# Kernel tuning notes

Hardware: AMD Instinct MI355X
Metric: run time of the kernel (lower is better)

The kernel has to match this reference:

```python
import jax, jax.numpy as jnp
import numpy as np

BETA = 0.25

def setup_inputs() -> dict:
    key = jax.random.key(0)
    k1, k2 = jax.random.split(key)
    z = jax.random.normal(k1, (4096, 64, 64), dtype=jnp.float32)
    codebooks = jax.random.normal(k2, (64, 256, 64), dtype=jnp.float32)
    return {"z": z, "codebooks": codebooks}

def reference(z, codebooks):
    # z: (B, M, d); codebooks: (M, K, d)
    B, M, d = z.shape
    # squared distances (B, M, K) via ||z||^2 - 2 z.c + ||c||^2 (avoids (B,M,K,d) blowup)
    z2 = jnp.sum(z * z, axis=-1)                      # (B, M)
    c2 = jnp.sum(codebooks * codebooks, axis=-1)      # (M, K)
    zc = jnp.einsum('bmd,mkd->bmk', z, codebooks)     # (B, M, K)
    distances = z2[:, :, None] - 2.0 * zc + c2[None]  # (B, M, K)
    encoding_indices = jnp.argmin(distances, axis=-1) # (B, M) int
    # per-subspace codebook gather: codebooks[m, idx[b, m], :]
    quantized_raw = codebooks[jnp.arange(M)[None, :], encoding_indices]  # (B, M, d)
    # straight-through estimator
    quantized = z + jax.lax.stop_gradient(quantized_raw - z)
    q_loss = (BETA * jnp.mean((jax.lax.stop_gradient(quantized) - z) ** 2)
              + jnp.mean((quantized - jax.lax.stop_gradient(z)) ** 2))
    return quantized, encoding_indices, q_loss
```

## Files before the change

kernel.cpp:

```cpp
#include <hip/hip_runtime.h>

#define IDX_BASE 16777216UL
#define LOSS_IDX 17039360UL
#define EPS2 0.02f

typedef float4 f4;
typedef _Float16 half8 __attribute__((ext_vector_type(8)));
typedef float f32x4 __attribute__((ext_vector_type(4)));

static __device__ __forceinline__ unsigned umax(unsigned a, unsigned b) { return a > b ? a : b; }
static __device__ __forceinline__ unsigned umin(unsigned a, unsigned b) { return a < b ? a : b; }
static __device__ __forceinline__ unsigned f2mono(float s) {
    unsigned u = __float_as_uint(s);
    return u ^ (unsigned)(((int)u >> 31) | 0x80000000);
}
static __device__ __forceinline__ float mono2f(unsigned v) {
    return __uint_as_float(v ^ (((unsigned)((int)(~v) >> 31)) | 0x80000000u));
}

__device__ __forceinline__ void gload_lds16(const float* g, float* s) {
    __builtin_amdgcn_global_load_lds(
        (const __attribute__((address_space(1))) unsigned int*)g,
        (__attribute__((address_space(3))) unsigned int*)s, 16, 0, 0);
}

__global__ __launch_bounds__(256) void pq_frag(const float* __restrict__ cb,
                                               half8* __restrict__ fragbuf,
                                               float* __restrict__ c2) {
    int bx = blockIdx.x, tid = threadIdx.x;
    int m = bx >> 2, sub = bx & 3;
    int w = tid >> 6, lane = tid & 63, lh = lane >> 4, l15 = lane & 15;
    const float* cbm = cb + (size_t)m * (256 * 64);
    half8* fbm = fragbuf + (size_t)m * (16 * 4 * 64);
    int tile = w * 4 + sub;
    int code = tile * 16 + l15;
    const float* crow = cbm + code * 64 + lh * 8;
    float ss = 0.f;
    #pragma unroll
    for (int s = 0; s < 2; ++s) {
        f4 a = *reinterpret_cast<const f4*>(crow + s * 32);
        f4 b = *reinterpret_cast<const f4*>(crow + s * 32 + 4);
        float v[8] = {a.x, a.y, a.z, a.w, b.x, b.y, b.z, b.w};
        half8 hi, lo;
        #pragma unroll
        for (int e = 0; e < 8; ++e) {
            _Float16 h = (_Float16)v[e];
            hi[e] = h; lo[e] = (_Float16)(v[e] - (float)h);
            ss = fmaf(v[e], v[e], ss);
        }
        fbm[(tile * 4 + s * 2 + 0) * 64 + lane] = hi;
        fbm[(tile * 4 + s * 2 + 1) * 64 + lane] = lo;
    }
    ss += __shfl_xor(ss, 16, 64);
    ss += __shfl_xor(ss, 32, 64);
    if (lh == 0) c2[m * 256 + code] = ss;
}

__global__ __launch_bounds__(256, 3) void pq_main(
    const float* __restrict__ z, const float* __restrict__ cb,
    const float* __restrict__ c2ws, const half8* __restrict__ fragbuf,
    float* __restrict__ out, float* __restrict__ partial)
{
    __shared__ f4       sZ4[128 * 16];
    __shared__ unsigned sK1[4 * 128];
    __shared__ unsigned sK2[4 * 128];
    __shared__ int      sBest[128];
    __shared__ float    sW[4];

    const int tid = threadIdx.x, bx = blockIdx.x;
    const int m = ((bx & 7) << 3) | ((bx >> 3) & 7);
    const int chunk = bx >> 6;
    const int w = tid >> 6, lane = tid & 63;
    const int lh = lane >> 4, l15 = lane & 15;
    const unsigned payBase = 255u - (unsigned)(w * 64 + lh * 4);

    const float* __restrict__ cbm = cb + (size_t)m * (256 * 64);
    const f4* cb4m = reinterpret_cast<const f4*>(cbm);

    #pragma unroll
    for (int i = 0; i < 8; ++i) {
        int unit = i * 256 + w * 64 + lane;
        int row = unit >> 4, c4 = unit & 15;
        int c4p = c4 ^ (row & 7);
        const float* src = z + ((size_t)(chunk * 128 + row) * 64 + m) * 64 + c4p * 4;
        gload_lds16(src, (float*)&sZ4[i * 256 + w * 64]);
    }

    const half8* __restrict__ fb = fragbuf + (size_t)m * (16 * 4 * 64);
    half8 ah[4][2], al[4][2];
    #pragma unroll
    for (int t = 0; t < 4; ++t) {
        #pragma unroll
        for (int s = 0; s < 2; ++s) {
            ah[t][s] = fb[((w * 4 + t) * 4 + s * 2 + 0) * 64 + lane];
            al[t][s] = fb[((w * 4 + t) * 4 + s * 2 + 1) * 64 + lane];
        }
    }
    const f4* __restrict__ c2t = reinterpret_cast<const f4*>(c2ws + m * 256);
    f32x4 c2i[4];
    #pragma unroll
    for (int t = 0; t < 4; ++t) {
        f4 cv = c2t[(w * 4 + t) * 4 + lh];
        c2i[t][0] = -0.5f*cv.x; c2i[t][1] = -0.5f*cv.y;
        c2i[t][2] = -0.5f*cv.z; c2i[t][3] = -0.5f*cv.w;
    }

    __syncthreads();

    #pragma unroll 1
    for (int rtp = 0; rtp < 4; ++rtp) {
        half8 bh0[2], bl0[2], bh1[2], bl1[2];
        #pragma unroll
        for (int h = 0; h < 2; ++h) {
            const int row = (rtp * 2 + h) * 16 + l15;
            const int swz = row & 7;
            const f4* zr = &sZ4[row * 16];
            const int c0 = lh << 1;
            f4 a0 = zr[(c0)     ^ swz];
            f4 a1 = zr[(c0 + 1) ^ swz];
            f4 a2 = zr[(c0 + 8) ^ swz];
            f4 a3 = zr[(c0 + 9) ^ swz];
            float v0[8] = {a0.x,a0.y,a0.z,a0.w,a1.x,a1.y,a1.z,a1.w};
            float v1[8] = {a2.x,a2.y,a2.z,a2.w,a3.x,a3.y,a3.z,a3.w};
            #pragma unroll
            for (int e = 0; e < 8; ++e) {
                _Float16 h0 = (_Float16)v0[e];
                bh0[h][e] = h0; bl0[h][e] = (_Float16)(v0[e] - (float)h0);
                _Float16 h1 = (_Float16)v1[e];
                bh1[h][e] = h1; bl1[h][e] = (_Float16)(v1[e] - (float)h1);
            }
        }
        unsigned K1[2] = {0u, 0u}, K2[2] = {0u, 0u};
        #pragma unroll
        for (int t = 0; t < 4; ++t) {
            const unsigned pb = payBase - (unsigned)(t * 16);
            #pragma unroll
            for (int h = 0; h < 2; ++h) {
                f32x4 acc = c2i[t];
                acc = __builtin_amdgcn_mfma_f32_16x16x32_f16(ah[t][0], bh0[h], acc, 0, 0, 0);
                acc = __builtin_amdgcn_mfma_f32_16x16x32_f16(ah[t][1], bh1[h], acc, 0, 0, 0);
                acc = __builtin_amdgcn_mfma_f32_16x16x32_f16(ah[t][0], bl0[h], acc, 0, 0, 0);
                acc = __builtin_amdgcn_mfma_f32_16x16x32_f16(ah[t][1], bl1[h], acc, 0, 0, 0);
                acc = __builtin_amdgcn_mfma_f32_16x16x32_f16(al[t][0], bh0[h], acc, 0, 0, 0);
                acc = __builtin_amdgcn_mfma_f32_16x16x32_f16(al[t][1], bh1[h], acc, 0, 0, 0);
                unsigned kk0 = (f2mono(acc[0]) & 0xFFFFFF00u) | (pb - 0u);
                unsigned kk1 = (f2mono(acc[1]) & 0xFFFFFF00u) | (pb - 1u);
                unsigned kk2 = (f2mono(acc[2]) & 0xFFFFFF00u) | (pb - 2u);
                unsigned kk3 = (f2mono(acc[3]) & 0xFFFFFF00u) | (pb - 3u);
                unsigned a  = umax(kk0, kk1), b2 = umin(kk0, kk1);
                unsigned c  = umax(kk2, kk3), d  = umin(kk2, kk3);
                unsigned t1 = umax(a, c);
                unsigned t2 = umax(umin(a, c), umax(b2, d));
                K2[h] = umax(umax(K2[h], t2), umin(K1[h], t1));
                K1[h] = umax(K1[h], t1);
            }
        }
        #pragma unroll
        for (int h = 0; h < 2; ++h) {
            #pragma unroll
            for (int off = 16; off <= 32; off <<= 1) {
                unsigned o1 = (unsigned)__shfl_xor((int)K1[h], off, 64);
                unsigned o2 = (unsigned)__shfl_xor((int)K2[h], off, 64);
                K2[h] = umax(umax(K2[h], o2), umin(K1[h], o1));
                K1[h] = umax(K1[h], o1);
            }
            if (lane < 16) {
                int r2 = (rtp * 2 + h) * 16 + lane;
                sK1[w * 128 + r2] = K1[h];
                sK2[w * 128 + r2] = K2[h];
            }
        }
    }
    __syncthreads();

    if (tid < 128) {
        unsigned G1 = 0u, G2 = 0u;
        #pragma unroll
        for (int w2 = 0; w2 < 4; ++w2) {
            unsigned k1w = sK1[w2 * 128 + tid];
            unsigned k2w = sK2[w2 * 128 + tid];
            G2 = umax(umax(G2, k2w), umin(G1, k1w));
            G1 = umax(G1, k1w);
        }
        float s1 = mono2f(G1 & 0xFFFFFF00u);
        float s2 = mono2f(G2 & 0xFFFFFF00u);
        sBest[tid] = (s1 - s2 < EPS2) ? -1 : (int)(255u - (G1 & 0xFFu));
    }
    __syncthreads();

    for (int row = w; row < 128; row += 4) {
        if (sBest[row] >= 0) continue;
        int swz = row & 7;
        float bs = -1e30f; int bk = 0;
        #pragma unroll 1
        for (int j = 0; j < 4; ++j) {
            int k = j * 64 + lane;
            float s = -0.5f * c2ws[m * 256 + k];
            #pragma unroll
            for (int d4 = 0; d4 < 16; ++d4) {
                f4 cvv = cb4m[k * 16 + d4];
                f4 zz  = sZ4[row * 16 + (d4 ^ swz)];
                s = fmaf(zz.x, cvv.x, s); s = fmaf(zz.y, cvv.y, s);
                s = fmaf(zz.z, cvv.z, s); s = fmaf(zz.w, cvv.w, s);
            }
            if (s > bs) { bs = s; bk = k; }
        }
        #pragma unroll
        for (int off = 1; off < 64; off <<= 1) {
            float ov = __shfl_xor(bs, off, 64);
            int   ok = __shfl_xor(bk, off, 64);
            if (ov > bs || (ov == bs && ok < bk)) { bs = ov; bk = ok; }
        }
        if (lane == 0) sBest[row] = bk;
    }
    __syncthreads();

    float lsum = 0.f;
    {
        int row = tid >> 1, h = tid & 1;
        int k = sBest[row];
        int b = chunk * 128 + row;
        int swz = row & 7;
        const f4* q4 = cb4m + (size_t)k * 16 + h * 8;
        f4*       o4 = reinterpret_cast<f4*>(out + ((size_t)b * 64 + m) * 64) + h * 8;
        float l0 = 0.f, l1 = 0.f;
        #pragma unroll
        for (int c = 0; c < 8; ++c) {
            f4 qv = q4[c];
            f4 zv = sZ4[row * 16 + (((h << 3) + c) ^ swz)];
            o4[c] = qv;
            float d0 = qv.x - zv.x, d1 = qv.y - zv.y, d2 = qv.z - zv.z, d3 = qv.w - zv.w;
            l0 = fmaf(d0, d0, l0); l1 = fmaf(d1, d1, l1);
            l0 = fmaf(d2, d2, l0); l1 = fmaf(d3, d3, l1);
        }
        lsum = l0 + l1;
    }
    if (tid < 128)
        out[IDX_BASE + (size_t)(chunk * 128 + tid) * 64 + m] = (float)sBest[tid];
    #pragma unroll
    for (int off = 1; off < 64; off <<= 1) lsum += __shfl_xor(lsum, off, 64);
    if (lane == 0) sW[w] = lsum;
    __syncthreads();
    if (tid == 0) partial[bx] = (sW[0] + sW[1]) + (sW[2] + sW[3]);
}

__global__ __launch_bounds__(256) void pq_loss(const float* __restrict__ partial,
                                               float* __restrict__ out)
{
    __shared__ float sW[4];
    float s = 0.f;
    #pragma unroll
    for (int i = 0; i < 8; ++i) s += partial[threadIdx.x + i * 256];
    #pragma unroll
    for (int off = 1; off < 64; off <<= 1) s += __shfl_xor(s, off, 64);
    if ((threadIdx.x & 63) == 0) sW[threadIdx.x >> 6] = s;
    __syncthreads();
    if (threadIdx.x == 0)
        out[LOSS_IDX] = ((sW[0] + sW[1]) + (sW[2] + sW[3])) * (1.25f / 16777216.0f);
}

extern "C" void kernel_launch(void* const* d_in, const int* in_sizes, int n_in,
                              void* d_out, int out_size, void* d_ws, size_t ws_size,
                              hipStream_t stream) {
    const float* zp  = (const float*)d_in[0];
    const float* cbp = (const float*)d_in[1];
    float* outp = (float*)d_out;
    float* c2ws = (float*)d_ws;
    half8* frag = (half8*)((float*)d_ws + 16384);
    float* part = (float*)d_ws + 16384 + 1048576;

    pq_frag<<<dim3(256),  dim3(256), 0, stream>>>(cbp, frag, c2ws);
    pq_main<<<dim3(2048), dim3(256), 0, stream>>>(zp, cbp, c2ws, frag, outp, part);
    pq_loss<<<dim3(1),    dim3(256), 0, stream>>>(part, outp);
}
```

Before: 84.58 us.

## Stage z as precomputed fp16 hi/lo MFMA fragments in LDS instead of fp32

Measured after the change: 94.01 us. +11.1%, slower.

```diff
diff --git a/kernel.cpp b/kernel.cpp
--- a/kernel.cpp
+++ b/kernel.cpp
@@ -16,12 +16,6 @@
 }
 static __device__ __forceinline__ float mono2f(unsigned v) {
     return __uint_as_float(v ^ (((unsigned)((int)(~v) >> 31)) | 0x80000000u));
-}
-
-__device__ __forceinline__ void gload_lds16(const float* g, float* s) {
-    __builtin_amdgcn_global_load_lds(
-        (const __attribute__((address_space(1))) unsigned int*)g,
-        (__attribute__((address_space(3))) unsigned int*)s, 16, 0, 0);
 }
 
 __global__ __launch_bounds__(256) void pq_frag(const float* __restrict__ cb,
@@ -61,7 +55,7 @@
     const float* __restrict__ c2ws, const half8* __restrict__ fragbuf,
     float* __restrict__ out, float* __restrict__ partial)
 {
-    __shared__ f4       sZ4[128 * 16];
+    __shared__ half8    sZfrag[8 * 4 * 64];
     __shared__ unsigned sK1[4 * 128];
     __shared__ unsigned sK2[4 * 128];
     __shared__ int      sBest[128];
@@ -78,12 +72,28 @@
     const f4* cb4m = reinterpret_cast<const f4*>(cbm);
 
     #pragma unroll
-    for (int i = 0; i < 8; ++i) {
-        int unit = i * 256 + w * 64 + lane;
-        int row = unit >> 4, c4 = unit & 15;
-        int c4p = c4 ^ (row & 7);
-        const float* src = z + ((size_t)(chunk * 128 + row) * 64 + m) * 64 + c4p * 4;
-        gload_lds16(src, (float*)&sZ4[i * 256 + w * 64]);
+    for (int i = 0; i < 2; ++i) {
+        int rt = w * 2 + i;
+        size_t rh = (size_t)(chunk * 128 + rt * 16 + l15);
+        const float* zb = z + (rh * 64 + m) * 64 + lh * 8;
+        f4 p0 = *reinterpret_cast<const f4*>(zb);
+        f4 p1 = *reinterpret_cast<const f4*>(zb + 4);
+        f4 p2 = *reinterpret_cast<const f4*>(zb + 32);
+        f4 p3 = *reinterpret_cast<const f4*>(zb + 36);
+        float v0[8] = {p0.x,p0.y,p0.z,p0.w,p1.x,p1.y,p1.z,p1.w};
+        float v1[8] = {p2.x,p2.y,p2.z,p2.w,p3.x,p3.y,p3.z,p3.w};
+        half8 h0, l0, h1, l1;
+        #pragma unroll
+        for (int e = 0; e < 8; ++e) {
+            _Float16 a = (_Float16)v0[e];
+            h0[e] = a; l0[e] = (_Float16)(v0[e] - (float)a);
+            _Float16 b = (_Float16)v1[e];
+            h1[e] = b; l1[e] = (_Float16)(v1[e] - (float)b);
+        }
+        sZfrag[rt * 256 +   0 + lane] = h0;
+        sZfrag[rt * 256 +  64 + lane] = l0;
+        sZfrag[rt * 256 + 128 + lane] = h1;
+        sZfrag[rt * 256 + 192 + lane] = l1;
     }
 
     const half8* __restrict__ fb = fragbuf + (size_t)m * (16 * 4 * 64);
@@ -108,67 +118,41 @@
     __syncthreads();
 
     #pragma unroll 1
-    for (int rtp = 0; rtp < 4; ++rtp) {
-        half8 bh0[2], bl0[2], bh1[2], bl1[2];
-        #pragma unroll
-        for (int h = 0; h < 2; ++h) {
-            const int row = (rtp * 2 + h) * 16 + l15;
-            const int swz = row & 7;
-            const f4* zr = &sZ4[row * 16];
-            const int c0 = lh << 1;
-            f4 a0 = zr[(c0)     ^ swz];
-            f4 a1 = zr[(c0 + 1) ^ swz];
-            f4 a2 = zr[(c0 + 8) ^ swz];
-            f4 a3 = zr[(c0 + 9) ^ swz];
-            float v0[8] = {a0.x,a0.y,a0.z,a0.w,a1.x,a1.y,a1.z,a1.w};
-            float v1[8] = {a2.x,a2.y,a2.z,a2.w,a3.x,a3.y,a3.z,a3.w};
-            #pragma unroll
-            for (int e = 0; e < 8; ++e) {
-                _Float16 h0 = (_Float16)v0[e];
-                bh0[h][e] = h0; bl0[h][e] = (_Float16)(v0[e] - (float)h0);
-                _Float16 h1 = (_Float16)v1[e];
-                bh1[h][e] = h1; bl1[h][e] = (_Float16)(v1[e] - (float)h1);
-            }
-        }
-        unsigned K1[2] = {0u, 0u}, K2[2] = {0u, 0u};
+    for (int rt = 0; rt < 8; ++rt) {
+        const half8* zf = &sZfrag[rt * 256 + lane];
+        half8 bh0 = zf[0], bl0 = zf[64], bh1 = zf[128], bl1 = zf[192];
+        unsigned K1 = 0u, K2 = 0u;
         #pragma unroll
         for (int t = 0; t < 4; ++t) {
             const unsigned pb = payBase - (unsigned)(t * 16);
-            #pragma unroll
-            for (int h = 0; h < 2; ++h) {
-                f32x4 acc = c2i[t];
-                acc = __builtin_amdgcn_mfma_f32_16x16x32_f16(ah[t][0], bh0[h], acc, 0, 0, 0);
-                acc = __builtin_amdgcn_mfma_f32_16x16x32_f16(ah[t][1], bh1[h], acc, 0, 0, 0);
-                acc = __builtin_amdgcn_mfma_f32_16x16x32_f16(ah[t][0], bl0[h], acc, 0, 0, 0);
-                acc = __builtin_amdgcn_mfma_f32_16x16x32_f16(ah[t][1], bl1[h], acc, 0, 0, 0);
-                acc = __builtin_amdgcn_mfma_f32_16x16x32_f16(al[t][0], bh0[h], acc, 0, 0, 0);
-                acc = __builtin_amdgcn_mfma_f32_16x16x32_f16(al[t][1], bh1[h], acc, 0, 0, 0);
-                unsigned kk0 = (f2mono(acc[0]) & 0xFFFFFF00u) | (pb - 0u);
-                unsigned kk1 = (f2mono(acc[1]) & 0xFFFFFF00u) | (pb - 1u);
-                unsigned kk2 = (f2mono(acc[2]) & 0xFFFFFF00u) | (pb - 2u);
-                unsigned kk3 = (f2mono(acc[3]) & 0xFFFFFF00u) | (pb - 3u);
-                unsigned a  = umax(kk0, kk1), b2 = umin(kk0, kk1);
-                unsigned c  = umax(kk2, kk3), d  = umin(kk2, kk3);
-                unsigned t1 = umax(a, c);
-                unsigned t2 = umax(umin(a, c), umax(b2, d));
-                K2[h] = umax(umax(K2[h], t2), umin(K1[h], t1));
-                K1[h] = umax(K1[h], t1);
-            }
-        }
-        #pragma unroll
-        for (int h = 0; h < 2; ++h) {
-            #pragma unroll
-            for (int off = 16; off <= 32; off <<= 1) {
-                unsigned o1 = (unsigned)__shfl_xor((int)K1[h], off, 64);
-                unsigned o2 = (unsigned)__shfl_xor((int)K2[h], off, 64);
-                K2[h] = umax(umax(K2[h], o2), umin(K1[h], o1));
-                K1[h] = umax(K1[h], o1);
-            }
-            if (lane < 16) {
-                int r2 = (rtp * 2 + h) * 16 + lane;
-                sK1[w * 128 + r2] = K1[h];
-                sK2[w * 128 + r2] = K2[h];
-            }
+            f32x4 acc = c2i[t];
+            acc = __builtin_amdgcn_mfma_f32_16x16x32_f16(ah[t][0], bh0, acc, 0, 0, 0);
+            acc = __builtin_amdgcn_mfma_f32_16x16x32_f16(ah[t][1], bh1, acc, 0, 0, 0);
+            acc = __builtin_amdgcn_mfma_f32_16x16x32_f16(ah[t][0], bl0, acc, 0, 0, 0);
+            acc = __builtin_amdgcn_mfma_f32_16x16x32_f16(ah[t][1], bl1, acc, 0, 0, 0);
+            acc = __builtin_amdgcn_mfma_f32_16x16x32_f16(al[t][0], bh0, acc, 0, 0, 0);
+            acc = __builtin_amdgcn_mfma_f32_16x16x32_f16(al[t][1], bh1, acc, 0, 0, 0);
+            unsigned kk0 = (f2mono(acc[0]) & 0xFFFFFF00u) | (pb - 0u);
+            unsigned kk1 = (f2mono(acc[1]) & 0xFFFFFF00u) | (pb - 1u);
+            unsigned kk2 = (f2mono(acc[2]) & 0xFFFFFF00u) | (pb - 2u);
+            unsigned kk3 = (f2mono(acc[3]) & 0xFFFFFF00u) | (pb - 3u);
+            unsigned a  = umax(kk0, kk1), b2 = umin(kk0, kk1);
+            unsigned c  = umax(kk2, kk3), d  = umin(kk2, kk3);
+            unsigned t1 = umax(a, c);
+            unsigned t2 = umax(umin(a, c), umax(b2, d));
+            K2 = umax(umax(K2, t2), umin(K1, t1));
+            K1 = umax(K1, t1);
+        }
+        #pragma unroll
+        for (int off = 16; off <= 32; off <<= 1) {
+            unsigned o1 = (unsigned)__shfl_xor((int)K1, off, 64);
+            unsigned o2 = (unsigned)__shfl_xor((int)K2, off, 64);
+            K2 = umax(umax(K2, o2), umin(K1, o1));
+            K1 = umax(K1, o1);
+        }
+        if (lane < 16) {
+            sK1[w * 128 + rt * 16 + lane] = K1;
+            sK2[w * 128 + rt * 16 + lane] = K2;
         }
     }
     __syncthreads();
@@ -190,7 +174,8 @@
 
     for (int row = w; row < 128; row += 4) {
         if (sBest[row] >= 0) continue;
-        int swz = row & 7;
+        size_t rg = (size_t)(chunk * 128 + row);
+        const f4* zr4 = reinterpret_cast<const f4*>(z + (rg * 64 + m) * 64);
         float bs = -1e30f; int bk = 0;
         #pragma unroll 1
         for (int j = 0; j < 4; ++j) {
@@ -199,7 +184,7 @@
             #pragma unroll
             for (int d4 = 0; d4 < 16; ++d4) {
                 f4 cvv = cb4m[k * 16 + d4];
-                f4 zz  = sZ4[row * 16 + (d4 ^ swz)];
+                f4 zz  = zr4[d4];
                 s = fmaf(zz.x, cvv.x, s); s = fmaf(zz.y, cvv.y, s);
                 s = fmaf(zz.z, cvv.z, s); s = fmaf(zz.w, cvv.w, s);
             }
@@ -217,17 +202,16 @@
 
     float lsum = 0.f;
     {
-        int row = tid >> 1, h = tid & 1;
+        int row = tid >> 1, hf = tid & 1;
         int k = sBest[row];
-        int b = chunk * 128 + row;
-        int swz = row & 7;
-        const f4* q4 = cb4m + (size_t)k * 16 + h * 8;
-        f4*       o4 = reinterpret_cast<f4*>(out + ((size_t)b * 64 + m) * 64) + h * 8;
+        size_t b = (size_t)(chunk * 128 + row);
+        const f4* q4 = cb4m + (size_t)k * 16 + hf * 8;
+        const f4* z4 = reinterpret_cast<const f4*>(z + (b * 64 + m) * 64) + hf * 8;
+        f4*       o4 = reinterpret_cast<f4*>(out + (b * 64 + m) * 64) + hf * 8;
         float l0 = 0.f, l1 = 0.f;
         #pragma unroll
         for (int c = 0; c < 8; ++c) {
-            f4 qv = q4[c];
-            f4 zv = sZ4[row * 16 + (((h << 3) + c) ^ swz)];
+            f4 qv = q4[c], zv = z4[c];
             o4[c] = qv;
             float d0 = qv.x - zv.x, d1 = qv.y - zv.y, d2 = qv.z - zv.z, d3 = qv.w - zv.w;
             l0 = fmaf(d0, d0, l0); l1 = fmaf(d1, d1, l1);
```
